# Kernel optimization log

Hardware: AMD Instinct MI355X
Metric: run time of the kernel (lower is better)

The kernel has to match this reference:

```python
import jax, jax.numpy as jnp
import numpy as np

B, T, H, NH = 4, 2048, 1024, 16
HD = H // NH  # 64


def setup_inputs() -> dict:
    key = jax.random.key(0)
    ks = jax.random.split(key, 8)
    s = 1.0 / np.sqrt(H)
    return {
        "hidden_states": jax.random.normal(ks[0], (B, T, H), dtype=jnp.float32),
        "attention_mask": jnp.zeros((B, 1, 1, T), dtype=jnp.float32),
        "Wq": jax.random.normal(ks[1], (H, H), dtype=jnp.float32) * s,
        "bq": jax.random.normal(ks[2], (H,), dtype=jnp.float32) * 0.01,
        "Wk": jax.random.normal(ks[3], (H, H), dtype=jnp.float32) * s,
        "bk": jax.random.normal(ks[4], (H,), dtype=jnp.float32) * 0.01,
        "Wv": jax.random.normal(ks[5], (H, H), dtype=jnp.float32) * s,
        "bv": jax.random.normal(ks[6], (H,), dtype=jnp.float32) * 0.01,
    }


def _split_heads(x):
    # [b, t, h*d] -> [b, h, t, d]
    b, t, _ = x.shape
    return x.reshape(b, t, NH, HD).transpose(0, 2, 1, 3)


def reference(hidden_states, attention_mask, Wq, bq, Wk, bk, Wv, bv):
    q = _split_heads(hidden_states @ Wq.T + bq)
    k = _split_heads(hidden_states @ Wk.T + bk)
    v = _split_heads(hidden_states @ Wv.T + bv)
    scores = jnp.einsum('bhqd,bhkd->bhqk', q, k) / jnp.sqrt(jnp.float32(HD))
    t = q.shape[2]
    causal = jnp.triu(jnp.ones((t, t), dtype=scores.dtype), k=1)[None, None] * (-1e9)
    scores = scores + causal + attention_mask
    probs = jax.nn.softmax(scores, axis=-1)
    # module returns [b, h, t, d] (no merge back)
    return jnp.einsum('bhqk,bhkd->bhqd', probs, v)
```

## Files before the change

### kernel.cpp

```cpp
#include <hip/hip_runtime.h>
#include <hip/hip_bf16.h>


typedef float  f32x4 __attribute__((ext_vector_type(4)));
typedef short  s16x8 __attribute__((ext_vector_type(8)));
typedef unsigned short u16;

#define LOG2E 1.44269504088896340736f

__device__ __forceinline__ u16 f2bf(float f) {
  unsigned u = __float_as_uint(f);
  u += 0x7FFFu + ((u >> 16) & 1u);
  return (u16)(u >> 16);
}
__device__ __forceinline__ float bf2f(u16 v) {
  return __uint_as_float(((unsigned)v) << 16);
}
__device__ __forceinline__ float ex2(float x) {
#if __has_builtin(__builtin_amdgcn_exp2f)
  return __builtin_amdgcn_exp2f(x);
#else
  return exp2f(x);
#endif
}
__device__ __forceinline__ float rcp_(float x) {
#if __has_builtin(__builtin_amdgcn_rcpf)
  return __builtin_amdgcn_rcpf(x);
#else
  return 1.0f / x;
#endif
}
__device__ __forceinline__ unsigned cvtpk(float lo, float hi) {
  unsigned r;
  asm("v_cvt_pk_bf16_f32 %0, %1, %2" : "=v"(r) : "v"(lo), "v"(hi));
  return r;
}
__device__ __forceinline__ void bar() {
  asm volatile("" ::: "memory");
  __builtin_amdgcn_s_barrier();
  asm volatile("" ::: "memory");
}

#define GLOAD16(gp, lp)                                                          \
  __builtin_amdgcn_global_load_lds(                                              \
      (const __attribute__((address_space(1))) void*)(gp),                       \
      (__attribute__((address_space(3))) void*)(lp), 16, 0, 0)

#define MFMA(a, b, c) __builtin_amdgcn_mfma_f32_16x16x32_bf16((a), (b), (c), 0, 0, 0)

__global__ __launch_bounds__(256) void cvt_all(
    const float* __restrict__ hs, const float* __restrict__ wq,
    const float* __restrict__ wk, const float* __restrict__ wv,
    const float* __restrict__ maskp,
    u16* __restrict__ xo, u16* __restrict__ qo, u16* __restrict__ ko,
    u16* __restrict__ vo, u16* __restrict__ wm) {
  int b = blockIdx.x;
  const float* s;
  u16* d;
  size_t i;
  bool isw = false;
  if (b < 4096) { s = hs; d = xo; i = (size_t)b * 256 + threadIdx.x; }
  else if (b < 5632) {
    int w = (b - 4096) >> 9, r = (b - 4096) & 511;
    s = (w == 0) ? wq : (w == 1) ? wk : wv;
    d = (w == 0) ? qo : (w == 1) ? ko : vo;
    i = (size_t)r * 256 + threadIdx.x;
  } else {
    s = maskp; d = wm; i = (size_t)(b - 5632) * 256 + threadIdx.x;
    isw = true;
  }
  const float4* sp = (const float4*)s + i * 2;
  float4 a = sp[0], c = sp[1];
  s16x8 r8;
  if (isw) {
    r8[0] = f2bf(ex2(a.x * LOG2E)); r8[1] = f2bf(ex2(a.y * LOG2E));
    r8[2] = f2bf(ex2(a.z * LOG2E)); r8[3] = f2bf(ex2(a.w * LOG2E));
    r8[4] = f2bf(ex2(c.x * LOG2E)); r8[5] = f2bf(ex2(c.y * LOG2E));
    r8[6] = f2bf(ex2(c.z * LOG2E)); r8[7] = f2bf(ex2(c.w * LOG2E));
  } else {
    r8[0] = f2bf(a.x); r8[1] = f2bf(a.y); r8[2] = f2bf(a.z); r8[3] = f2bf(a.w);
    r8[4] = f2bf(c.x); r8[5] = f2bf(c.y); r8[6] = f2bf(c.z); r8[7] = f2bf(c.w);
  }
  *(s16x8*)(d + i * 8) = r8;
}

__global__ __launch_bounds__(512, 2) void qkv_gemm(
    const u16* __restrict__ Xb,
    const u16* __restrict__ Wqb, const u16* __restrict__ Wkb,
    const u16* __restrict__ Wvb,
    const float* __restrict__ bq, const float* __restrict__ bk,
    const float* __restrict__ bv, const u16* __restrict__ Wm,
    u16* __restrict__ Qo, u16* __restrict__ Ko, u16* __restrict__ Vto) {
  int bid0 = blockIdx.x;
  int bid  = (bid0 & 7) * 96 + (bid0 >> 3);
  int which = bid % 3;
  int rt = bid / 3;
  int mt = rt >> 3, nt = rt & 7;
  const u16* W = (which == 0) ? Wqb : (which == 1) ? Wkb : Wvb;
  const float* bias = (which == 0) ? bq : (which == 1) ? bk : bv;

  __shared__ __align__(16) char lds[98304];

  int tid = threadIdx.x;
  int lane = tid & 63, wid = tid >> 6;
  int q16 = lane & 15, g = lane >> 4;
  int wr = wid >> 1, wc = wid & 1;

  int srow = tid >> 3, sslot = tid & 7;
  int sw = (sslot ^ (srow & 7)) << 4;
  const char* Asrc = (const char*)Xb + (size_t)(mt * 256 + srow) * 2048 + sw;
  const char* Bsrc = (const char*)W  + (size_t)(nt * 128 + srow) * 2048 + sw;

  int slot0 = (g ^ (q16 & 7)) << 4;

#define STAGE_AB(tt, buf) do { size_t so = (size_t)(tt) * 128;                   \
    GLOAD16(Asrc + so,          lds + (buf) * 32768 + tid * 16);                 \
    GLOAD16(Asrc + so + 131072, lds + (buf) * 32768 + 8192 + tid * 16);          \
    GLOAD16(Asrc + so + 262144, lds + (buf) * 32768 + 16384 + tid * 16);         \
    GLOAD16(Asrc + so + 393216, lds + (buf) * 32768 + 24576 + tid * 16);         \
    GLOAD16(Bsrc + so,          lds + 65536 + (buf) * 16384 + tid * 16);         \
    GLOAD16(Bsrc + so + 131072, lds + 65536 + (buf) * 16384 + 8192 + tid * 16); } while (0)

#define LDA(FA, buf, mp) do {                                                    \
    const char* p_ = lds + (buf) * 32768 + (wr * 64 + (mp) * 32 + q16) * 128;    \
    FA[0] = *(const s16x8*)(p_ + slot0);                                         \
    FA[1] = *(const s16x8*)(p_ + (slot0 ^ 64));                                  \
    FA[2] = *(const s16x8*)(p_ + 2048 + slot0);                                  \
    FA[3] = *(const s16x8*)(p_ + 2048 + (slot0 ^ 64)); } while (0)

#define LDB(FB, buf) do {                                                        \
    const char* p_ = lds + 65536 + (buf) * 16384 + (wc * 64 + q16) * 128;        \
    FB[0] = *(const s16x8*)(p_ + slot0);                                         \
    FB[1] = *(const s16x8*)(p_ + (slot0 ^ 64));                                  \
    FB[2] = *(const s16x8*)(p_ + 2048 + slot0);                                  \
    FB[3] = *(const s16x8*)(p_ + 2048 + (slot0 ^ 64));                           \
    FB[4] = *(const s16x8*)(p_ + 4096 + slot0);                                  \
    FB[5] = *(const s16x8*)(p_ + 4096 + (slot0 ^ 64));                           \
    FB[6] = *(const s16x8*)(p_ + 6144 + slot0);                                  \
    FB[7] = *(const s16x8*)(p_ + 6144 + (slot0 ^ 64)); } while (0)

#define MM16(mlo, FA, FB) do {                                                   \
    _Pragma("unroll")                                                            \
    for (int n_ = 0; n_ < 4; ++n_) {                                             \
      acc[(mlo)][n_]     = MFMA(FA[0], FB[2 * n_],     acc[(mlo)][n_]);          \
      acc[(mlo)][n_]     = MFMA(FA[1], FB[2 * n_ + 1], acc[(mlo)][n_]);          \
      acc[(mlo) + 1][n_] = MFMA(FA[2], FB[2 * n_],     acc[(mlo) + 1][n_]);      \
      acc[(mlo) + 1][n_] = MFMA(FA[3], FB[2 * n_ + 1], acc[(mlo) + 1][n_]);      \
    } } while (0)

  STAGE_AB(0, 0);

  f32x4 acc[4][4] = {};
  s16x8 fA0[4], fA1[4], fB[8];

#pragma unroll 1
  for (int i = 0; i < 16; ++i) {
    int buf = i & 1;
    if (i < 15) {
      STAGE_AB(i + 1, buf ^ 1);
      asm volatile("s_waitcnt vmcnt(6)" ::: "memory");
    } else {
      asm volatile("s_waitcnt vmcnt(0)" ::: "memory");
    }
    bar();
    LDA(fA0, buf, 0);
    LDA(fA1, buf, 1);
    LDB(fB, buf);
    __builtin_amdgcn_s_setprio(1);
    MM16(0, fA0, fB);
    MM16(2, fA1, fB);
    __builtin_amdgcn_s_setprio(0);
    bar();
  }

  u16* tile = (u16*)(void*)lds + (size_t)wid * 64 * 72;
  int h0 = nt * 2 + wc;
  int m_base = mt * 256 + wr * 64;
  int bb = m_base >> 11;
  int t0 = m_base & 2047;

  if (which != 2) {
    float qsc = (which == 0) ? (0.125f * LOG2E) : 1.0f;
#pragma unroll
    for (int n = 0; n < 4; ++n) {
      float bvl = bias[h0 * 64 + n * 16 + q16];
#pragma unroll
      for (int m = 0; m < 4; ++m)
#pragma unroll
        for (int j = 0; j < 4; ++j)
          tile[(m * 16 + g * 4 + j) * 72 + n * 16 + q16] =
              f2bf((acc[m][n][j] + bvl) * qsc);
    }
  } else {
    const u16* wrow = Wm + (size_t)bb * 2048 + t0;
    float wv[4][4];
#pragma unroll
    for (int m = 0; m < 4; ++m)
#pragma unroll
      for (int j = 0; j < 4; ++j)
        wv[m][j] = bf2f(wrow[m * 16 + g * 4 + j]);
#pragma unroll
    for (int n = 0; n < 4; ++n) {
      float bvl = bias[h0 * 64 + n * 16 + q16];
#pragma unroll
      for (int m = 0; m < 4; ++m)
#pragma unroll
        for (int j = 0; j < 4; ++j)
          tile[(n * 16 + q16) * 72 + m * 16 + g * 4 + j] =
              f2bf((acc[m][n][j] + bvl) * wv[m][j]);
    }
  }
  asm volatile("" ::: "memory");

  const char* tb = (const char*)tile;
  int rl = lane >> 3, cb = (lane & 7) * 16;
  if (which != 2) {
    u16* Out = (which == 0) ? Qo : Ko;
    char* gbase = (char*)(Out + ((size_t)(bb * 16 + h0) * 2048 + t0) * 64);
#pragma unroll
    for (int c = 0; c < 8; ++c) {
      int row = rl + c * 8;
      s16x8 v = *(const s16x8*)(tb + row * 144 + cb);
      *(s16x8*)(gbase + row * 128 + cb) = v;
    }
  } else {
    char* gbase = (char*)Vto + ((size_t)(bb * 16 + h0) * 64) * 4096 + t0 * 2;
#pragma unroll
    for (int c = 0; c < 8; ++c) {
      int d = rl + c * 8;
      s16x8 v = *(const s16x8*)(tb + d * 144 + cb);
      *(s16x8*)(gbase + (size_t)d * 4096 + cb) = v;
    }
  }
#undef STAGE_AB
#undef LDA
#undef LDB
#undef MM16
}

__global__ __launch_bounds__(256, 2) void attn_fwd(
    const u16* __restrict__ Qw, const u16* __restrict__ Kw,
    const u16* __restrict__ Vtw, const u16* __restrict__ Wm,
    float* __restrict__ out) {
  int bid0 = blockIdx.x;
  int bid = (bid0 & 7) * 64 + (bid0 >> 3);
  int bh = bid >> 3, p = bid & 7;
  int tid = threadIdx.x;
  int lane = tid & 63, wid = tid >> 6;
  int q16 = lane & 15, g = lane >> 4;

  __shared__ __align__(16) char Ks[3][8192];
  __shared__ __align__(16) char Vs[3][8192];
  __shared__ __align__(16) u16 wl[2048];

  int srow = tid >> 3;
  int sinner = (tid & 7) << 4;
  int fs = (srow & 7) ^ ((srow >> 1) & 4);
  int ssw = sinner ^ (fs << 4);
  const char* Kg = (const char*)Kw + ((size_t)bh * 2048 + srow) * 128 + ssw;
  const char* Vg = (const char*)Vtw + ((size_t)bh * 64 + srow) * 4096 + ssw;

#define STAGE_T(kt, b) do {                                                      \
    GLOAD16(Kg + (size_t)(kt) * 8192,        Ks[b] + tid * 16);                  \
    GLOAD16(Kg + (size_t)(kt) * 8192 + 4096, Ks[b] + tid * 16 + 4096);           \
    GLOAD16(Vg + (size_t)(kt) * 128,          Vs[b] + tid * 16);                 \
    GLOAD16(Vg + (size_t)(kt) * 128 + 131072, Vs[b] + tid * 16 + 4096); } while (0)

  GLOAD16((const char*)Wm + (size_t)(bh >> 4) * 4096 + tid * 16,
          (char*)wl + tid * 16);

  auto run_phase = [&](int qtl) {
    int nt = 2 * qtl + 2;
    int qw0 = (qtl << 7) + wid * 32;
    size_t qr = (size_t)bh * 2048 + qw0 + q16;
    s16x8 qa[2][2];
#pragma unroll
    for (int h = 0; h < 2; ++h) {
      qa[h][0] = *(const s16x8*)(Qw + (qr + 16 * h) * 64 + g * 8);
      qa[h][1] = *(const s16x8*)(Qw + (qr + 16 * h) * 64 + 32 + g * 8);
    }
    STAGE_T(0, 0);
    STAGE_T(1, 1);

    f32x4 o[2][4] = {};
    f32x4 lw[2] = {};
    int bc = 0;

#pragma unroll 1
    for (int kt = 0; kt < nt; ++kt) {
      if (kt + 2 < nt) {
        int bp = bc + 2; if (bp >= 3) bp -= 3;
        STAGE_T(kt + 2, bp);
        asm volatile("s_waitcnt vmcnt(8)" ::: "memory");
      } else if (kt + 1 < nt) {
        asm volatile("s_waitcnt vmcnt(4)" ::: "memory");
      } else {
        asm volatile("s_waitcnt vmcnt(0)" ::: "memory");
      }
      __builtin_amdgcn_s_barrier();
      asm volatile("" ::: "memory");

      if (64 * kt <= qw0 + 31) {
        int kb = kt << 6;
        const char* ksb = Ks[bc];
        const char* vsb = Vs[bc];
        bool causal = (64 * kt + 63 > qw0);
#pragma unroll
        for (int c = 0; c < 2; ++c) {
          f32x4 sA[2][2];
          __builtin_amdgcn_s_setprio(1);
#pragma unroll
          for (int t4 = 0; t4 < 2; ++t4) {
            int kk = 32 * c + ((q16 >> 2) << 3) + (t4 << 2) + (q16 & 3);
            int fk = (kk & 7) ^ ((kk >> 1) & 4);
            const char* krow = ksb + kk * 128;
            int in0 = (g * 16) ^ (fk << 4);
            s16x8 kf0 = *(const s16x8*)(krow + in0);
            s16x8 kf1 = *(const s16x8*)(krow + (in0 ^ 64));
#pragma unroll
            for (int h = 0; h < 2; ++h) {
              f32x4 sv = {0.f, 0.f, 0.f, 0.f};
              sv = MFMA(kf0, qa[h][0], sv);
              sv = MFMA(kf1, qa[h][1], sv);
              sA[t4][h] = sv;
            }
          }
          __builtin_amdgcn_s_setprio(0);

          s16x8 wf = *(const s16x8*)((const char*)wl + (kb + 32 * c + 8 * g) * 2);

          union { s16x8 v; unsigned u[4]; } pb[2];
#pragma unroll
          for (int h = 0; h < 2; ++h) {
            int qc = qw0 + 16 * h + q16;
#pragma unroll
            for (int t4 = 0; t4 < 2; ++t4) {
              float a0 = ex2(sA[t4][h][0]), a1 = ex2(sA[t4][h][1]);
              float a2 = ex2(sA[t4][h][2]), a3 = ex2(sA[t4][h][3]);
              if (causal) {
                int k0 = kb + 32 * c + 8 * g + 4 * t4;
                a0 = (k0 + 0 <= qc) ? a0 : 0.f;
                a1 = (k0 + 1 <= qc) ? a1 : 0.f;
                a2 = (k0 + 2 <= qc) ? a2 : 0.f;
                a3 = (k0 + 3 <= qc) ? a3 : 0.f;
              }
              pb[h].u[t4 * 2 + 0] = cvtpk(a0, a1);
              pb[h].u[t4 * 2 + 1] = cvtpk(a2, a3);
            }
          }

          __builtin_amdgcn_s_setprio(1);
#pragma unroll
          for (int dt = 0; dt < 4; ++dt) {
            int d = dt * 16 + q16;
            int fv = (d & 7) ^ ((d >> 1) & 4);
            s16x8 vf = *(const s16x8*)(vsb + d * 128 + ((64 * c + 16 * g) ^ (fv << 4)));
#pragma unroll
            for (int h = 0; h < 2; ++h)
              o[h][dt] = MFMA(vf, pb[h].v, o[h][dt]);
          }
#pragma unroll
          for (int h = 0; h < 2; ++h)
            lw[h] = MFMA(wf, pb[h].v, lw[h]);
          __builtin_amdgcn_s_setprio(0);
        }
      }
      __builtin_amdgcn_s_barrier();
      asm volatile("" ::: "memory");
      if (++bc >= 3) bc -= 3;
    }

#pragma unroll
    for (int h = 0; h < 2; ++h) {
      float inv = rcp_(lw[h][0]);
      float* op = out + ((size_t)bh * 2048 + qw0 + 16 * h + q16) * 64 + g * 4;
#pragma unroll
      for (int dt = 0; dt < 4; ++dt)
        *(f32x4*)(op + dt * 16) = o[h][dt] * inv;
    }
  };

  run_phase(15 - p);
  run_phase(p);
#undef STAGE_T
}

extern "C" void kernel_launch(void* const* d_in, const int* in_sizes, int n_in,
                              void* d_out, int out_size, void* d_ws, size_t ws_size,
                              hipStream_t stream) {
  const float* hs   = (const float*)d_in[0];
  const float* mask = (const float*)d_in[1];
  const float* Wq   = (const float*)d_in[2];
  const float* bq   = (const float*)d_in[3];
  const float* Wk   = (const float*)d_in[4];
  const float* bk   = (const float*)d_in[5];
  const float* Wv   = (const float*)d_in[6];
  const float* bv   = (const float*)d_in[7];
  float* out = (float*)d_out;

  char* w = (char*)d_ws;
  u16* Xb  = (u16*)w; w += (size_t)8192 * 1024 * 2;
  u16* Wqb = (u16*)w; w += (size_t)1024 * 1024 * 2;
  u16* Wkb = (u16*)w; w += (size_t)1024 * 1024 * 2;
  u16* Wvb = (u16*)w; w += (size_t)1024 * 1024 * 2;
  u16* Qw  = (u16*)w; w += (size_t)8192 * 1024 * 2;
  u16* Kw  = (u16*)w; w += (size_t)8192 * 1024 * 2;
  u16* Vtw = (u16*)w; w += (size_t)8192 * 1024 * 2;
  u16* Wm  = (u16*)w; w += (size_t)8192 * 2;

  cvt_all<<<5636, 256, 0, stream>>>(hs, Wq, Wk, Wv, mask, Xb, Wqb, Wkb, Wvb, Wm);
  qkv_gemm<<<768, 512, 0, stream>>>(Xb, Wqb, Wkb, Wvb, bq, bk, bv, Wm, Qw, Kw, Vtw);
  attn_fwd<<<512, 256, 0, stream>>>(Qw, Kw, Vtw, Wm, out);
}
```

Measured before the change: 134.1 us.

## Enlarge QKV GEMM tile to 256x256 with finer-grained interleaved staging

The QKV projection GEMM moves from 256x128 block tiles to 256x256 tiles, halving the grid to 384 blocks. Each wave now owns a 128x64 output tile. The main loop is split into four sub-phases that interleave global-to-LDS loads with MFMA groups. The aim is higher arithmetic intensity and fewer redundant reads of the activation matrix. In exchange, LDS grows to 128KB, accumulator registers double, and the single fewer wave of blocks may hurt occupancy and tail balance on 256 CUs.

```diff
diff --git a/kernel.cpp b/kernel.cpp
--- a/kernel.cpp
+++ b/kernel.cpp
@@ -92,150 +92,154 @@
     const float* __restrict__ bv, const u16* __restrict__ Wm,
     u16* __restrict__ Qo, u16* __restrict__ Ko, u16* __restrict__ Vto) {
   int bid0 = blockIdx.x;
-  int bid  = (bid0 & 7) * 96 + (bid0 >> 3);
+  int bid  = (bid0 & 7) * 48 + (bid0 >> 3);
   int which = bid % 3;
   int rt = bid / 3;
-  int mt = rt >> 3, nt = rt & 7;
+  int mt = rt >> 2, nt = rt & 3;
   const u16* W = (which == 0) ? Wqb : (which == 1) ? Wkb : Wvb;
   const float* bias = (which == 0) ? bq : (which == 1) ? bk : bv;
 
-  __shared__ __align__(16) char lds[98304];
+  __shared__ __align__(16) char lds[131072];
 
   int tid = threadIdx.x;
   int lane = tid & 63, wid = tid >> 6;
   int q16 = lane & 15, g = lane >> 4;
-  int wr = wid >> 1, wc = wid & 1;
-
-  int srow = tid >> 3, sslot = tid & 7;
-  int sw = (sslot ^ (srow & 7)) << 4;
-  const char* Asrc = (const char*)Xb + (size_t)(mt * 256 + srow) * 2048 + sw;
-  const char* Bsrc = (const char*)W  + (size_t)(nt * 128 + srow) * 2048 + sw;
+  int wr = wid >> 2, wc = wid & 3;
+
+  int rloc = tid >> 3;
+  int sw = ((tid & 7) ^ (rloc & 7)) << 4;
+  const char* Asrc = (const char*)Xb + (size_t)(mt * 256 + rloc) * 2048 + sw;
+  const char* Bsrc = (const char*)W  + (size_t)(nt * 256 + rloc) * 2048 + sw;
 
   int slot0 = (g ^ (q16 & 7)) << 4;
 
-#define STAGE_AB(tt, buf) do { size_t so = (size_t)(tt) * 128;                   \
-    GLOAD16(Asrc + so,          lds + (buf) * 32768 + tid * 16);                 \
-    GLOAD16(Asrc + so + 131072, lds + (buf) * 32768 + 8192 + tid * 16);          \
-    GLOAD16(Asrc + so + 262144, lds + (buf) * 32768 + 16384 + tid * 16);         \
-    GLOAD16(Asrc + so + 393216, lds + (buf) * 32768 + 24576 + tid * 16);         \
-    GLOAD16(Bsrc + so,          lds + 65536 + (buf) * 16384 + tid * 16);         \
-    GLOAD16(Bsrc + so + 131072, lds + 65536 + (buf) * 16384 + 8192 + tid * 16); } while (0)
-
-#define LDA(FA, buf, mp) do {                                                    \
-    const char* p_ = lds + (buf) * 32768 + (wr * 64 + (mp) * 32 + q16) * 128;    \
-    FA[0] = *(const s16x8*)(p_ + slot0);                                         \
-    FA[1] = *(const s16x8*)(p_ + (slot0 ^ 64));                                  \
-    FA[2] = *(const s16x8*)(p_ + 2048 + slot0);                                  \
-    FA[3] = *(const s16x8*)(p_ + 2048 + (slot0 ^ 64)); } while (0)
-
-#define LDB(FB, buf) do {                                                        \
-    const char* p_ = lds + 65536 + (buf) * 16384 + (wc * 64 + q16) * 128;        \
-    FB[0] = *(const s16x8*)(p_ + slot0);                                         \
-    FB[1] = *(const s16x8*)(p_ + (slot0 ^ 64));                                  \
-    FB[2] = *(const s16x8*)(p_ + 2048 + slot0);                                  \
-    FB[3] = *(const s16x8*)(p_ + 2048 + (slot0 ^ 64));                           \
-    FB[4] = *(const s16x8*)(p_ + 4096 + slot0);                                  \
-    FB[5] = *(const s16x8*)(p_ + 4096 + (slot0 ^ 64));                           \
-    FB[6] = *(const s16x8*)(p_ + 6144 + slot0);                                  \
-    FB[7] = *(const s16x8*)(p_ + 6144 + (slot0 ^ 64)); } while (0)
-
-#define MM16(mlo, FA, FB) do {                                                   \
+#define SA(u, h) do { size_t so = (size_t)(u) * 128 + (size_t)(h) * 262144;      \
+    char* dd = lds + ((u) & 1) * 32768 + (h) * 16384 + tid * 16;                 \
+    GLOAD16(Asrc + so, dd);                                                      \
+    GLOAD16(Asrc + so + 131072, dd + 8192); } while (0)
+#define SB(u, h) do { size_t so = (size_t)(u) * 128 + (size_t)(h) * 262144;      \
+    char* dd = lds + 65536 + ((u) & 1) * 32768 + (h) * 16384 + tid * 16;         \
+    GLOAD16(Bsrc + so, dd);                                                      \
+    GLOAD16(Bsrc + so + 131072, dd + 8192); } while (0)
+
+#define LDA8(kh, buf) do {                                                       \
+    const char* p_ = lds + (buf) * 32768 + (wr * 128 + q16) * 128 +              \
+                     (slot0 ^ ((kh) * 64));                                      \
     _Pragma("unroll")                                                            \
-    for (int n_ = 0; n_ < 4; ++n_) {                                             \
-      acc[(mlo)][n_]     = MFMA(FA[0], FB[2 * n_],     acc[(mlo)][n_]);          \
-      acc[(mlo)][n_]     = MFMA(FA[1], FB[2 * n_ + 1], acc[(mlo)][n_]);          \
-      acc[(mlo) + 1][n_] = MFMA(FA[2], FB[2 * n_],     acc[(mlo) + 1][n_]);      \
-      acc[(mlo) + 1][n_] = MFMA(FA[3], FB[2 * n_ + 1], acc[(mlo) + 1][n_]);      \
-    } } while (0)
-
-  STAGE_AB(0, 0);
-
-  f32x4 acc[4][4] = {};
-  s16x8 fA0[4], fA1[4], fB[8];
+    for (int m_ = 0; m_ < 8; ++m_) fA[m_] = *(const s16x8*)(p_ + m_ * 2048); } while (0)
+
+#define LDB2(nh, kh, buf) do {                                                   \
+    const char* p_ = lds + 65536 + (buf) * 32768 +                               \
+                     (wc * 64 + (nh) * 32 + q16) * 128 + (slot0 ^ ((kh) * 64));  \
+    fB[0] = *(const s16x8*)(p_);                                                 \
+    fB[1] = *(const s16x8*)(p_ + 2048); } while (0)
+
+#define MM(nh) do {                                                              \
+    __builtin_amdgcn_s_setprio(1);                                               \
+    _Pragma("unroll")                                                            \
+    for (int m_ = 0; m_ < 8; ++m_) {                                             \
+      acc[m_][2 * (nh)]     = MFMA(fA[m_], fB[0], acc[m_][2 * (nh)]);            \
+      acc[m_][2 * (nh) + 1] = MFMA(fA[m_], fB[1], acc[m_][2 * (nh) + 1]);        \
+    }                                                                            \
+    __builtin_amdgcn_s_setprio(0); } while (0)
+
+  SA(0, 0); SA(0, 1); SB(0, 0); SB(0, 1);
+  SA(1, 0);
+  asm volatile("s_waitcnt vmcnt(2)" ::: "memory");
+  bar();
+
+  f32x4 acc[8][4] = {};
+  s16x8 fA[8], fB[2];
 
 #pragma unroll 1
-  for (int i = 0; i < 16; ++i) {
-    int buf = i & 1;
-    if (i < 15) {
-      STAGE_AB(i + 1, buf ^ 1);
-      asm volatile("s_waitcnt vmcnt(6)" ::: "memory");
-    } else {
+  for (int t = 0; t < 16; ++t) {
+    int buf = t & 1;
+    LDA8(0, buf); LDB2(0, 0, buf);
+    if (t < 15) SA(t + 1, 1);
+    bar(); MM(0); bar();
+    LDB2(1, 0, buf);
+    if (t < 15) SB(t + 1, 0);
+    bar(); MM(1); bar();
+    LDA8(1, buf); LDB2(0, 1, buf);
+    if (t < 15) SB(t + 1, 1);
+    bar(); MM(0); bar();
+    LDB2(1, 1, buf);
+    if (t < 14) {
+      SA(t + 2, 0);
+      asm volatile("s_waitcnt vmcnt(2)" ::: "memory");
+    } else if (t == 14) {
       asm volatile("s_waitcnt vmcnt(0)" ::: "memory");
     }
-    bar();
-    LDA(fA0, buf, 0);
-    LDA(fA1, buf, 1);
-    LDB(fB, buf);
-    __builtin_amdgcn_s_setprio(1);
-    MM16(0, fA0, fB);
-    MM16(2, fA1, fB);
-    __builtin_amdgcn_s_setprio(0);
-    bar();
+    bar(); MM(1); bar();
   }
 
-  u16* tile = (u16*)(void*)lds + (size_t)wid * 64 * 72;
-  int h0 = nt * 2 + wc;
-  int m_base = mt * 256 + wr * 64;
-  int bb = m_base >> 11;
-  int t0 = m_base & 2047;
-
-  if (which != 2) {
-    float qsc = (which == 0) ? (0.125f * LOG2E) : 1.0f;
-#pragma unroll
-    for (int n = 0; n < 4; ++n) {
-      float bvl = bias[h0 * 64 + n * 16 + q16];
-#pragma unroll
-      for (int m = 0; m < 4; ++m)
-#pragma unroll
-        for (int j = 0; j < 4; ++j)
-          tile[(m * 16 + g * 4 + j) * 72 + n * 16 + q16] =
-              f2bf((acc[m][n][j] + bvl) * qsc);
-    }
-  } else {
-    const u16* wrow = Wm + (size_t)bb * 2048 + t0;
-    float wv[4][4];
-#pragma unroll
-    for (int m = 0; m < 4; ++m)
-#pragma unroll
-      for (int j = 0; j < 4; ++j)
-        wv[m][j] = bf2f(wrow[m * 16 + g * 4 + j]);
-#pragma unroll
-    for (int n = 0; n < 4; ++n) {
-      float bvl = bias[h0 * 64 + n * 16 + q16];
-#pragma unroll
-      for (int m = 0; m < 4; ++m)
-#pragma unroll
-        for (int j = 0; j < 4; ++j)
-          tile[(n * 16 + q16) * 72 + m * 16 + g * 4 + j] =
-              f2bf((acc[m][n][j] + bvl) * wv[m][j]);
-    }
-  }
-  asm volatile("" ::: "memory");
-
+  float qsc = (which == 0) ? (0.125f * LOG2E) : 1.0f;
+  u16* Out = (which == 0) ? Qo : (which == 1) ? Ko : Vto;
+  int h0 = nt * 4 + wc;
+  u16* tile = (u16*)(void*)lds + (size_t)wid * 4608;
   const char* tb = (const char*)tile;
   int rl = lane >> 3, cb = (lane & 7) * 16;
-  if (which != 2) {
-    u16* Out = (which == 0) ? Qo : Ko;
-    char* gbase = (char*)(Out + ((size_t)(bb * 16 + h0) * 2048 + t0) * 64);
-#pragma unroll
-    for (int c = 0; c < 8; ++c) {
-      int row = rl + c * 8;
-      s16x8 v = *(const s16x8*)(tb + row * 144 + cb);
-      *(s16x8*)(gbase + row * 128 + cb) = v;
-    }
-  } else {
-    char* gbase = (char*)Vto + ((size_t)(bb * 16 + h0) * 64) * 4096 + t0 * 2;
-#pragma unroll
-    for (int c = 0; c < 8; ++c) {
-      int d = rl + c * 8;
-      s16x8 v = *(const s16x8*)(tb + d * 144 + cb);
-      *(s16x8*)(gbase + (size_t)d * 4096 + cb) = v;
-    }
+
+#pragma unroll 1
+  for (int p = 0; p < 2; ++p) {
+    int mbase = mt * 256 + wr * 128 + p * 64;
+    int bb = mbase >> 11, t0 = mbase & 2047;
+    if (which != 2) {
+#pragma unroll
+      for (int n = 0; n < 4; ++n) {
+        float bvl = bias[h0 * 64 + n * 16 + q16];
+#pragma unroll
+        for (int mm = 0; mm < 4; ++mm)
+#pragma unroll
+          for (int j = 0; j < 4; ++j)
+            tile[(mm * 16 + g * 4 + j) * 72 + n * 16 + q16] =
+                f2bf((acc[p * 4 + mm][n][j] + bvl) * qsc);
+      }
+    } else {
+      const u16* wrow = Wm + (size_t)bb * 2048 + t0;
+      float wv[4][4];
+#pragma unroll
+      for (int mm = 0; mm < 4; ++mm)
+#pragma unroll
+        for (int j = 0; j < 4; ++j)
+          wv[mm][j] = bf2f(wrow[mm * 16 + g * 4 + j]);
+#pragma unroll
+      for (int n = 0; n < 4; ++n) {
+        float bvl = bias[h0 * 64 + n * 16 + q16];
+#pragma unroll
+        for (int mm = 0; mm < 4; ++mm)
+#pragma unroll
+          for (int j = 0; j < 4; ++j)
+            tile[(n * 16 + q16) * 72 + mm * 16 + g * 4 + j] =
+                f2bf((acc[p * 4 + mm][n][j] + bvl) * wv[mm][j]);
+      }
+    }
+    asm volatile("" ::: "memory");
+
+    if (which != 2) {
+      char* gbase = (char*)(Out + ((size_t)(bb * 16 + h0) * 2048 + t0) * 64);
+#pragma unroll
+      for (int c = 0; c < 8; ++c) {
+        int row = rl + c * 8;
+        s16x8 v = *(const s16x8*)(tb + row * 144 + cb);
+        *(s16x8*)(gbase + row * 128 + cb) = v;
+      }
+    } else {
+      char* gbase = (char*)Out + ((size_t)(bb * 16 + h0) * 64) * 4096 + t0 * 2;
+#pragma unroll
+      for (int c = 0; c < 8; ++c) {
+        int d = rl + c * 8;
+        s16x8 v = *(const s16x8*)(tb + d * 144 + cb);
+        *(s16x8*)(gbase + (size_t)d * 4096 + cb) = v;
+      }
+    }
+    asm volatile("" ::: "memory");
   }
-#undef STAGE_AB
-#undef LDA
-#undef LDB
-#undef MM16
+#undef SA
+#undef SB
+#undef LDA8
+#undef LDB2
+#undef MM
 }
 
 __global__ __launch_bounds__(256, 2) void attn_fwd(
@@ -409,6 +413,6 @@
   u16* Wm  = (u16*)w; w += (size_t)8192 * 2;
 
   cvt_all<<<5636, 256, 0, stream>>>(hs, Wq, Wk, Wv, mask, Xb, Wqb, Wkb, Wvb, Wm);
-  qkv_gemm<<<768, 512, 0, stream>>>(Xb, Wqb, Wkb, Wvb, bq, bk, bv, Wm, Qw, Kw, Vtw);
+  qkv_gemm<<<384, 512, 0, stream>>>(Xb, Wqb, Wkb, Wvb, bq, bk, bv, Wm, Qw, Kw, Vtw);
   attn_fwd<<<512, 256, 0, stream>>>(Qw, Kw, Vtw, Wm, out);
 }
```

After: 184.8 us. 1.38x slower.
